# Kernel optimization log

Measured on AMD Instinct MI355X. Metric: run time of the kernel, lower is better.

Reference implementation:

```python
import jax, jax.numpy as jnp
import numpy as np

EMB_DIM = 1024
HEAD_SIZE = 128
B, T = 8, 2048


def setup_inputs() -> dict:
    key = jax.random.key(0)
    kx, kk, kq, kv = jax.random.split(key, 4)
    x = jax.random.normal(kx, (B, T, EMB_DIM), dtype=jnp.float32)
    # torch nn.Linear(emb_dim, head_size, bias=False): weight [head_size, emb_dim], y = x @ W.T
    # store transposed as [emb_dim, head_size] for direct matmul
    s = 1.0 / np.sqrt(EMB_DIM)
    Wk = jax.random.uniform(kk, (EMB_DIM, HEAD_SIZE), dtype=jnp.float32, minval=-s, maxval=s)
    Wq = jax.random.uniform(kq, (EMB_DIM, HEAD_SIZE), dtype=jnp.float32, minval=-s, maxval=s)
    Wv = jax.random.uniform(kv, (EMB_DIM, HEAD_SIZE), dtype=jnp.float32, minval=-s, maxval=s)
    return {"x": x, "Wk": Wk, "Wq": Wq, "Wv": Wv}


def reference(x, Wk, Wq, Wv):
    Bb, Tt, C = x.shape
    k = jnp.einsum('btc,ch->bth', x, Wk)
    q = jnp.einsum('btc,ch->bth', x, Wq)
    v = jnp.einsum('btc,ch->bth', x, Wv)
    # NOTE: original computes k @ q^T (not q @ k^T) and scales by C**-0.5 (C = emb_dim)
    wei = jnp.einsum('bih,bjh->bij', k, q) * (C ** -0.5)  # [B, T, T]
    causal = jnp.tril(jnp.ones((Tt, Tt), dtype=bool))
    wei = jnp.where(causal, wei, -jnp.inf)
    wei = jax.nn.softmax(wei, axis=-1)
    out = jnp.einsum('bij,bjh->bih', wei, v)  # [B, T, head_size]
    return out
```

## Files before the change

### kernel.cpp

```cpp
#include <hip/hip_runtime.h>
#include <hip/hip_bf16.h>
#include <stdint.h>

#define Bn 8
#define Tn 2048
#define Cn 1024
#define Hn 128

typedef __attribute__((ext_vector_type(8))) short short8;
typedef __attribute__((ext_vector_type(4))) short short4v;
typedef __attribute__((ext_vector_type(4))) float f32x4;
typedef __attribute__((ext_vector_type(4))) int int4v;

static __device__ __forceinline__ unsigned short f2bf(float f) {
    union { float f; unsigned int u; } v; v.f = f;
    return (unsigned short)((v.u + 0x7FFFu + ((v.u >> 16) & 1u)) >> 16);
}
static __device__ __forceinline__ float bf2f(unsigned short h) {
    union { unsigned int u; float f; } v; v.u = ((unsigned int)h) << 16;
    return v.f;
}

static __device__ __forceinline__ short8 cvt8(f32x4 a, f32x4 b) {
    union { unsigned int u[4]; short8 s; } r;
    asm("v_cvt_pk_bf16_f32 %0, %1, %2" : "=v"(r.u[0]) : "v"(a[0]), "v"(a[1]));
    asm("v_cvt_pk_bf16_f32 %0, %1, %2" : "=v"(r.u[1]) : "v"(a[2]), "v"(a[3]));
    asm("v_cvt_pk_bf16_f32 %0, %1, %2" : "=v"(r.u[2]) : "v"(b[0]), "v"(b[1]));
    asm("v_cvt_pk_bf16_f32 %0, %1, %2" : "=v"(r.u[3]) : "v"(b[2]), "v"(b[3]));
    return r.s;
}

static __device__ __forceinline__ void async16(const void* g, void* l) {
    __builtin_amdgcn_global_load_lds(
        (const __attribute__((address_space(1))) unsigned int*)g,
        (__attribute__((address_space(3))) unsigned int*)l,
        16, 0, 0);
}

#define KSCALE 0.04508422f

#define BASE_BYTES (3u * Bn * Tn * Hn * 2u + 3u * Hn * Cn * 2u)
#define SLOT_SH 2080
#define NBLK_FA 576
#define UPB_FA 72
#define CCHUNK 8

__global__ __launch_bounds__(256) void wt_prep(const float* __restrict__ Wk,
                                               const float* __restrict__ Wq,
                                               const float* __restrict__ Wv,
                                               unsigned short* __restrict__ WT) {
    int z = blockIdx.y;
    const float* W = (z == 0) ? Wk : (z == 1) ? Wq : Wv;
    unsigned short* wt = WT + (size_t)z * Hn * Cn;
    int o = blockIdx.x * 256 + threadIdx.x;
    int d = o >> 10;
    int k = o & (Cn - 1);
    wt[o] = f2bf(W[k * Hn + d]);
}

__global__ __launch_bounds__(256) void proj6(const float* __restrict__ x,
                                             const unsigned short* __restrict__ WTb,
                                             unsigned short* __restrict__ Kb,
                                             unsigned short* __restrict__ Qb,
                                             unsigned short* __restrict__ VT) {
    __shared__ __align__(16) unsigned short Bsm[2][128 * 32];
    __shared__ __align__(16) float Asm[2][64 * 32];
    int tid = threadIdx.x;
    int lane = tid & 63, w = tid >> 6;
    int lr = lane & 15, lg = lane >> 4;
    int wm = w >> 1, wn = w & 1;

    int u = ((int)(blockIdx.x & 7)) * 96 + ((int)blockIdx.x >> 3);
    int rg = u / 3, cg = u - rg * 3;
    int r0 = rg * 64;
    const unsigned short* WTz = WTb + (size_t)cg * Hn * Cn;

    int br_in = lane >> 2;
    int bc8 = (lane & 3) * 8;
    int ar_in = lane >> 3;
    int aspos = lane & 7;

    auto STAGE = [&](int bb, int k0) {
        #pragma unroll
        for (int i = 0; i < 2; ++i) {
            int ch = w * 2 + i;
            int brow = ch * 16 + br_in;
            async16(WTz + (size_t)brow * Cn + k0 + bc8, &Bsm[bb][ch * 512]);
            int arow = ch * 8 + ar_in;
            int ac = aspos ^ (arow & 7);
            async16(x + (size_t)(r0 + arow) * Cn + k0 + ac * 4, &Asm[bb][ch * 256]);
        }
    };

    f32x4 acc[2][4] = {};
    STAGE(0, 0);
    __syncthreads();
    int cur = 0;
    for (int ks = 0; ks < 32; ++ks) {
        if (ks < 31) STAGE(cur ^ 1, (ks + 1) * 32);
        short8 af[2], bf[4];
        #pragma unroll
        for (int m = 0; m < 2; ++m) {
            int arow = wm * 32 + m * 16 + lr;
            const char* abase = (const char*)&Asm[cur][arow * 32];
            f32x4 a0 = *(const f32x4*)(abase + ((((lg * 2)    ) ^ (arow & 7)) << 4));
            f32x4 a1 = *(const f32x4*)(abase + ((((lg * 2) + 1) ^ (arow & 7)) << 4));
            af[m] = cvt8(a0, a1);
        }
        #pragma unroll
        for (int c = 0; c < 4; ++c) {
            int brow = wn * 64 + c * 16 + lr;
            bf[c] = *(const short8*)(&Bsm[cur][brow * 32 + lg * 8]);
        }
        #pragma unroll
        for (int m = 0; m < 2; ++m)
            #pragma unroll
            for (int c = 0; c < 4; ++c)
                acc[m][c] = __builtin_amdgcn_mfma_f32_16x16x32_bf16(af[m], bf[c], acc[m][c], 0, 0, 0);
        __syncthreads();
        cur ^= 1;
    }

    if (cg == 2) {
        int bb = r0 >> 11;
        int tb = r0 & 2047;
        #pragma unroll
        for (int m = 0; m < 2; ++m)
            #pragma unroll
            for (int c = 0; c < 4; ++c) {
                int d = wn * 64 + c * 16 + lr;
                int t = tb + wm * 32 + m * 16 + lg * 4;
                short4v pv;
                pv[0] = (short)f2bf(acc[m][c][0]);
                pv[1] = (short)f2bf(acc[m][c][1]);
                pv[2] = (short)f2bf(acc[m][c][2]);
                pv[3] = (short)f2bf(acc[m][c][3]);
                *(short4v*)(VT + ((size_t)(bb * Hn + d) << 11) + t) = pv;
            }
    } else {
        unsigned short* outp = (cg == 0) ? Kb : Qb;
        float sc = (cg == 0) ? KSCALE : 1.0f;
        #pragma unroll
        for (int m = 0; m < 2; ++m)
            #pragma unroll
            for (int c = 0; c < 4; ++c) {
                int d = wn * 64 + c * 16 + lr;
                #pragma unroll
                for (int r = 0; r < 4; ++r) {
                    int i = r0 + wm * 32 + m * 16 + lg * 4 + r;
                    outp[(size_t)i * Hn + d] = f2bf(acc[m][c][r] * sc);
                }
            }
    }
}

__global__ __launch_bounds__(512) void fattn8(const unsigned short* __restrict__ Kb,
                                              const unsigned short* __restrict__ Qb,
                                              const unsigned short* __restrict__ VT,
                                              unsigned short* __restrict__ accP) {
    __shared__ __align__(16) unsigned short Ksm[2][32 * 128];
    __shared__ __align__(16) unsigned short Vsm[2][128 * 32];
    __shared__ __align__(16) unsigned short pbuf[8][16][48];
    int tid = threadIdx.x, lane = tid & 63, w = tid >> 6;
    int lr = lane & 15, lg = lane >> 4;

    int cpx = gridDim.x >> 3;
    int u = ((int)blockIdx.x & 7) * cpx + ((int)blockIdx.x >> 3);
    int b = u / UPB_FA, rem = u - b * UPB_FA;
    int g = 0, p = 0;
    for (;;) {
        int P = (4 * g + 4 + CCHUNK - 1) / CCHUNK;
        if (rem < P) { p = rem; break; }
        rem -= P; ++g;
    }
    int nt = 4 * g + 4;
    int P = (nt + CCHUNK - 1) / CCHUNK;
    int q = nt / P, r = nt % P;
    int begin = p * q + (p < r ? p : r);
    int size = q + (p < r ? 1 : 0);

    int i0 = g * 128 + w * 16;
    int tmax = (i0 + 15) >> 5;
    const unsigned short* kb = Kb + (size_t)b * Tn * Hn;
    const unsigned short* qb = Qb + (size_t)b * Tn * Hn;
    const unsigned short* vt = VT + (size_t)b * Hn * Tn;

    short8 kf[4];
    #pragma unroll
    for (int kk = 0; kk < 4; ++kk)
        kf[kk] = *(const short8*)(kb + (size_t)(i0 + lr) * Hn + kk * 32 + lg * 8);

    int krow = tid >> 4, kcol = (tid & 15) * 8;
    int vrow = tid >> 2, vcol = (tid & 3) * 8;
    int4v kreg, vreg;
    auto LOADT = [&](int tt) {
        int j0 = tt * 32;
        kreg = *(const int4v*)(qb + (size_t)(j0 + krow) * Hn + kcol);
        vreg = *(const int4v*)(vt + (size_t)vrow * Tn + j0 + vcol);
    };
    auto WRITET = [&](int bb) {
        *(int4v*)((char*)&Ksm[bb][0] + krow * 256 + ((kcol * 2) ^ ((krow & 7) << 4))) = kreg;
        *(int4v*)((char*)&Vsm[bb][0] + vrow * 64 + vcol * 2) = vreg;
    };

    f32x4 acc[8] = {};
    float ssum[4] = {0.f, 0.f, 0.f, 0.f};

    LOADT(begin);
    WRITET(0);
    __syncthreads();
    int cur = 0;
    for (int ti = 0; ti < size; ++ti) {
        int tt = begin + ti;
        if (ti + 1 < size) LOADT(tt + 1);
        if (tt <= tmax) {
            int j0 = tt * 32;
            const char* kbp = (const char*)&Ksm[cur][0];
            const char* vbp = (const char*)&Vsm[cur][0];
            f32x4 sa0 = {}, sa1 = {};
            #pragma unroll
            for (int kk = 0; kk < 4; ++kk) {
                int row = lr;
                short8 qf = *(const short8*)(kbp + row * 256 + (((kk * 64) + lg * 16) ^ ((row & 7) << 4)));
                sa0 = __builtin_amdgcn_mfma_f32_16x16x32_bf16(kf[kk], qf, sa0, 0, 0, 0);
            }
            #pragma unroll
            for (int kk = 0; kk < 4; ++kk) {
                int row = 16 + lr;
                short8 qf = *(const short8*)(kbp + row * 256 + (((kk * 64) + lg * 16) ^ ((row & 7) << 4)));
                sa1 = __builtin_amdgcn_mfma_f32_16x16x32_bf16(kf[kk], qf, sa1, 0, 0, 0);
            }
            bool needmask = (j0 + 31 > i0);
            #pragma unroll
            for (int rr = 0; rr < 4; ++rr) {
                float v0 = sa0[rr], v1 = sa1[rr];
                if (needmask) {
                    int i = i0 + lg * 4 + rr;
                    if (j0 + lr > i)      v0 = -1e30f;
                    if (j0 + 16 + lr > i) v1 = -1e30f;
                }
                float p0 = __builtin_amdgcn_exp2f(v0);
                float p1 = __builtin_amdgcn_exp2f(v1);
                ssum[rr] += p0 + p1;
                pbuf[w][lg * 4 + rr][lr] = f2bf(p0);
                pbuf[w][lg * 4 + rr][16 + lr] = f2bf(p1);
            }
            short8 pf = *(const short8*)(&pbuf[w][lr][lg * 8]);
            #pragma unroll
            for (int n = 0; n < 8; ++n) {
                int row = n * 16 + lr;
                short8 vf = *(const short8*)(vbp + row * 64 + lg * 16);
                acc[n] = __builtin_amdgcn_mfma_f32_16x16x32_bf16(pf, vf, acc[n], 0, 0, 0);
            }
        }
        if (ti + 1 < size) WRITET(cur ^ 1);
        __syncthreads();
        cur ^= 1;
    }

    unsigned short* dst = accP + (size_t)u * 8 * SLOT_SH + (size_t)w * SLOT_SH;
    #pragma unroll
    for (int n = 0; n < 8; ++n) {
        short4v pv;
        pv[0] = (short)f2bf(acc[n][0]);
        pv[1] = (short)f2bf(acc[n][1]);
        pv[2] = (short)f2bf(acc[n][2]);
        pv[3] = (short)f2bf(acc[n][3]);
        *(short4v*)(dst + n * 256 + lane * 4) = pv;
    }
    #pragma unroll
    for (int rr = 0; rr < 4; ++rr) {
        float s = ssum[rr];
        s += __shfl_xor(s, 1);
        s += __shfl_xor(s, 2);
        s += __shfl_xor(s, 4);
        s += __shfl_xor(s, 8);
        if (lr == 0) ((float*)(dst + 2048))[lg * 4 + rr] = s;
    }
}

__global__ __launch_bounds__(256) void combine3(const unsigned short* __restrict__ accP,
                                                float* __restrict__ out) {
    int cpx = gridDim.x >> 3;
    int bidx = ((int)blockIdx.x & 7) * cpx + ((int)blockIdx.x >> 3);
    int b = bidx >> 7, tile = bidx & 127;
    int g = tile >> 3, wq = tile & 7;
    int ub = b * UPB_FA;
    for (int gg = 0; gg < g; ++gg) ub += (4 * gg + 4 + CCHUNK - 1) / CCHUNK;
    int nt = 4 * g + 4;
    int P = (nt + CCHUNK - 1) / CCHUNK;

    int tid = threadIdx.x;
    int row = tid >> 4;
    int c8 = (tid & 15) * 8;

    const unsigned short* base = accP + ((size_t)ub * 8 + wq) * SLOT_SH;
    const size_t pstr = (size_t)8 * SLOT_SH;
    float den = 0.f;
    for (int pp = 0; pp < P; ++pp) den += ((const float*)(base + pp * pstr + 2048))[row];
    float inv = 1.0f / den;

    int lgg = row >> 2, r4 = row & 3;
    float ov[8];
    #pragma unroll
    for (int cc = 0; cc < 8; ++cc) {
        int col = c8 + cc;
        int n = col >> 4, lrr = col & 15;
        int flat = n * 256 + (lgg * 16 + lrr) * 4 + r4;
        float s = 0.f;
        for (int pp = 0; pp < P; ++pp) s += bf2f(base[pp * pstr + flat]);
        ov[cc] = s * inv;
    }
    float* op = out + ((size_t)(b * Tn + tile * 16 + row)) * Hn + c8;
    *(f32x4*)op       = f32x4{ov[0], ov[1], ov[2], ov[3]};
    *(f32x4*)(op + 4) = f32x4{ov[4], ov[5], ov[6], ov[7]};
}

__global__ __launch_bounds__(256) void attn(const unsigned short* __restrict__ Kb,
                                            const unsigned short* __restrict__ Qb,
                                            const unsigned short* __restrict__ VT,
                                            float* __restrict__ out) {
    __shared__ unsigned short pbuf[4][16][32];
    __shared__ __align__(16) float accbuf[4][16][132];
    __shared__ float ssbuf[4][16];
    int lane = threadIdx.x & 63;
    int w = threadIdx.x >> 6;
    int b = blockIdx.y;
    int xb = blockIdx.x;
    int tile = (xb & 1) ? (127 - (xb >> 1)) : (xb >> 1);
    int i0 = tile * 16;
    int lr = lane & 15, lg = lane >> 4;

    const unsigned short* kb = Kb + (size_t)b * Tn * Hn;
    const unsigned short* qb = Qb + (size_t)b * Tn * Hn;
    const unsigned short* vt = VT + (size_t)b * Hn * Tn;

    short8 kf[4];
    #pragma unroll
    for (int kk = 0; kk < 4; ++kk)
        kf[kk] = *(const short8*)(kb + (size_t)(i0 + lr) * Hn + kk * 32 + lg * 8);

    f32x4 acc[8] = {};
    float ssum[4] = {0.f, 0.f, 0.f, 0.f};

    int nt = (i0 + 15) / 32 + 1;
    for (int tt = w; tt < nt; tt += 4) {
        int j0 = tt * 32;
        f32x4 sa0 = {}, sa1 = {};
        #pragma unroll
        for (int kk = 0; kk < 4; ++kk) {
            short8 q0 = *(const short8*)(qb + (size_t)(j0 + lr) * Hn + kk * 32 + lg * 8);
            sa0 = __builtin_amdgcn_mfma_f32_16x16x32_bf16(kf[kk], q0, sa0, 0, 0, 0);
        }
        #pragma unroll
        for (int kk = 0; kk < 4; ++kk) {
            short8 q1 = *(const short8*)(qb + (size_t)(j0 + 16 + lr) * Hn + kk * 32 + lg * 8);
            sa1 = __builtin_amdgcn_mfma_f32_16x16x32_bf16(kf[kk], q1, sa1, 0, 0, 0);
        }
        bool needmask = (j0 + 31 > i0);
        #pragma unroll
        for (int r = 0; r < 4; ++r) {
            float v0 = sa0[r], v1 = sa1[r];
            if (needmask) {
                int i = i0 + lg * 4 + r;
                if (j0 + lr > i)      v0 = -1e30f;
                if (j0 + 16 + lr > i) v1 = -1e30f;
            }
            float p0 = __builtin_amdgcn_exp2f(v0);
            float p1 = __builtin_amdgcn_exp2f(v1);
            ssum[r] += p0 + p1;
            pbuf[w][lg * 4 + r][lr] = f2bf(p0);
            pbuf[w][lg * 4 + r][16 + lr] = f2bf(p1);
        }
        short8 pf = *(const short8*)(&pbuf[w][lr][lg * 8]);
        #pragma unroll
        for (int n = 0; n < 8; ++n) {
            short8 vf = *(const short8*)(vt + (size_t)(n * 16 + lr) * Tn + j0 + lg * 8);
            acc[n] = __builtin_amdgcn_mfma_f32_16x16x32_bf16(pf, vf, acc[n], 0, 0, 0);
        }
    }

    #pragma unroll
    for (int r = 0; r < 4; ++r) {
        float s = ssum[r];
        s += __shfl_xor(s, 1);
        s += __shfl_xor(s, 2);
        s += __shfl_xor(s, 4);
        s += __shfl_xor(s, 8);
        if (lr == 0) ssbuf[w][lg * 4 + r] = s;
    }
    #pragma unroll
    for (int n = 0; n < 8; ++n)
        #pragma unroll
        for (int r = 0; r < 4; ++r)
            accbuf[w][lg * 4 + r][n * 16 + lr] = acc[n][r];
    __syncthreads();

    int row = threadIdx.x >> 5;
    int col = (threadIdx.x & 31) * 4;
    #pragma unroll
    for (int h = 0; h < 2; ++h) {
        int rr = row + h * 8;
        f32x4 s = *(const f32x4*)(&accbuf[0][rr][col]);
        #pragma unroll
        for (int ww = 1; ww < 4; ++ww) {
            f32x4 t = *(const f32x4*)(&accbuf[ww][rr][col]);
            s[0] += t[0]; s[1] += t[1]; s[2] += t[2]; s[3] += t[3];
        }
        float den = ssbuf[0][rr] + ssbuf[1][rr] + ssbuf[2][rr] + ssbuf[3][rr];
        float inv = 1.0f / den;
        s[0] *= inv; s[1] *= inv; s[2] *= inv; s[3] *= inv;
        *(f32x4*)(&out[((size_t)(b * Tn + i0 + rr)) * Hn + col]) = s;
    }
}

extern "C" void kernel_launch(void* const* d_in, const int* in_sizes, int n_in,
                              void* d_out, int out_size, void* d_ws, size_t ws_size,
                              hipStream_t stream) {
    const float* x  = (const float*)d_in[0];
    const float* Wk = (const float*)d_in[1];
    const float* Wq = (const float*)d_in[2];
    const float* Wv = (const float*)d_in[3];

    unsigned short* Kb = (unsigned short*)d_ws;
    unsigned short* Qb = Kb + (size_t)Bn * Tn * Hn;
    unsigned short* VT = Qb + (size_t)Bn * Tn * Hn;
    unsigned short* WT = VT + (size_t)Bn * Tn * Hn;
    unsigned short* accP = (unsigned short*)((char*)d_ws + BASE_BYTES);

    wt_prep<<<dim3(512, 3), 256, 0, stream>>>(Wk, Wq, Wv, WT);
    proj6<<<dim3(768), 256, 0, stream>>>(x, WT, Kb, Qb, VT);

    const size_t need = (size_t)BASE_BYTES + (size_t)NBLK_FA * 8 * SLOT_SH * 2;
    if (ws_size >= need) {
        fattn8<<<dim3(NBLK_FA), 512, 0, stream>>>(Kb, Qb, VT, accP);
        combine3<<<dim3(1024), 256, 0, stream>>>(accP, (float*)d_out);
    } else {
        attn<<<dim3(128, 8), 256, 0, stream>>>(Kb, Qb, VT, (float*)d_out);
    }
}
```

Baseline: 83.47 us.

## Load x via registers, convert to bf16 once into LDS, double K-step to 64

```diff
diff --git a/kernel.cpp b/kernel.cpp
--- a/kernel.cpp
+++ b/kernel.cpp
@@ -58,13 +58,13 @@
     wt[o] = f2bf(W[k * Hn + d]);
 }
 
-__global__ __launch_bounds__(256) void proj6(const float* __restrict__ x,
+__global__ __launch_bounds__(256) void proj7(const float* __restrict__ x,
                                              const unsigned short* __restrict__ WTb,
                                              unsigned short* __restrict__ Kb,
                                              unsigned short* __restrict__ Qb,
                                              unsigned short* __restrict__ VT) {
-    __shared__ __align__(16) unsigned short Bsm[2][128 * 32];
-    __shared__ __align__(16) float Asm[2][64 * 32];
+    __shared__ __align__(16) unsigned short Bsm[2][128 * 64];
+    __shared__ __align__(16) unsigned short Asm[2][64 * 64];
     int tid = threadIdx.x;
     int lane = tid & 63, w = tid >> 6;
     int lr = lane & 15, lg = lane >> 4;
@@ -75,48 +75,74 @@
     int r0 = rg * 64;
     const unsigned short* WTz = WTb + (size_t)cg * Hn * Cn;
 
-    int br_in = lane >> 2;
-    int bc8 = (lane & 3) * 8;
-    int ar_in = lane >> 3;
-    int aspos = lane & 7;
-
-    auto STAGE = [&](int bb, int k0) {
-        #pragma unroll
-        for (int i = 0; i < 2; ++i) {
-            int ch = w * 2 + i;
-            int brow = ch * 16 + br_in;
-            async16(WTz + (size_t)brow * Cn + k0 + bc8, &Bsm[bb][ch * 512]);
-            int arow = ch * 8 + ar_in;
-            int ac = aspos ^ (arow & 7);
-            async16(x + (size_t)(r0 + arow) * Cn + k0 + ac * 4, &Asm[bb][ch * 256]);
-        }
+    int brow_in = lane >> 3;
+    int bslot = (lane & 7) ^ brow_in;
+    const unsigned short* bsrc[4];
+    #pragma unroll
+    for (int i = 0; i < 4; ++i) {
+        int ch = w * 4 + i;
+        bsrc[i] = WTz + (size_t)(ch * 8 + brow_in) * Cn + bslot * 8;
+    }
+
+    int ar_s = tid >> 2;
+    int ah = tid & 3;
+    const float* axp = x + (size_t)(r0 + ar_s) * Cn + ah * 16;
+    int asw = (ar_s & 7) << 4;
+    unsigned int awb0 = ar_s * 128 + ((ah * 32) ^ asw);
+    unsigned int awb1 = ar_s * 128 + ((ah * 32 + 16) ^ asw);
+
+    f32x4 a_r[4];
+    auto LOADA = [&](int k0) {
+        #pragma unroll
+        for (int i = 0; i < 4; ++i)
+            a_r[i] = *(const f32x4*)(axp + k0 + i * 4);
     };
+    auto STAGEB = [&](int bb, int k0) {
+        #pragma unroll
+        for (int i = 0; i < 4; ++i)
+            async16(bsrc[i] + k0, &Bsm[bb][(w * 4 + i) * 512]);
+    };
+    auto WRITEA = [&](int bb) {
+        short8 w0 = cvt8(a_r[0], a_r[1]);
+        short8 w1 = cvt8(a_r[2], a_r[3]);
+        char* base = (char*)&Asm[bb][0];
+        *(short8*)(base + awb0) = w0;
+        *(short8*)(base + awb1) = w1;
+    };
 
     f32x4 acc[2][4] = {};
-    STAGE(0, 0);
+    LOADA(0);
+    STAGEB(0, 0);
+    WRITEA(0);
     __syncthreads();
     int cur = 0;
-    for (int ks = 0; ks < 32; ++ks) {
-        if (ks < 31) STAGE(cur ^ 1, (ks + 1) * 32);
-        short8 af[2], bf[4];
-        #pragma unroll
-        for (int m = 0; m < 2; ++m) {
-            int arow = wm * 32 + m * 16 + lr;
-            const char* abase = (const char*)&Asm[cur][arow * 32];
-            f32x4 a0 = *(const f32x4*)(abase + ((((lg * 2)    ) ^ (arow & 7)) << 4));
-            f32x4 a1 = *(const f32x4*)(abase + ((((lg * 2) + 1) ^ (arow & 7)) << 4));
-            af[m] = cvt8(a0, a1);
-        }
-        #pragma unroll
-        for (int c = 0; c < 4; ++c) {
-            int brow = wn * 64 + c * 16 + lr;
-            bf[c] = *(const short8*)(&Bsm[cur][brow * 32 + lg * 8]);
-        }
-        #pragma unroll
-        for (int m = 0; m < 2; ++m)
-            #pragma unroll
-            for (int c = 0; c < 4; ++c)
-                acc[m][c] = __builtin_amdgcn_mfma_f32_16x16x32_bf16(af[m], bf[c], acc[m][c], 0, 0, 0);
+    for (int ks = 0; ks < 16; ++ks) {
+        if (ks < 15) {
+            LOADA((ks + 1) * 64);
+            STAGEB(cur ^ 1, (ks + 1) * 64);
+        }
+        const char* ab = (const char*)&Asm[cur][0];
+        const char* bbp = (const char*)&Bsm[cur][0];
+        #pragma unroll
+        for (int kk = 0; kk < 2; ++kk) {
+            short8 af[2], bf[4];
+            #pragma unroll
+            for (int m = 0; m < 2; ++m) {
+                int row = wm * 32 + m * 16 + lr;
+                af[m] = *(const short8*)(ab + row * 128 + ((kk * 64 + lg * 16) ^ ((row & 7) << 4)));
+            }
+            #pragma unroll
+            for (int c = 0; c < 4; ++c) {
+                int row = wn * 64 + c * 16 + lr;
+                bf[c] = *(const short8*)(bbp + row * 128 + ((kk * 64 + lg * 16) ^ ((row & 7) << 4)));
+            }
+            #pragma unroll
+            for (int m = 0; m < 2; ++m)
+                #pragma unroll
+                for (int c = 0; c < 4; ++c)
+                    acc[m][c] = __builtin_amdgcn_mfma_f32_16x16x32_bf16(af[m], bf[c], acc[m][c], 0, 0, 0);
+        }
+        if (ks < 15) WRITEA(cur ^ 1);
         __syncthreads();
         cur ^= 1;
     }
@@ -429,7 +455,7 @@
     unsigned short* accP = (unsigned short*)((char*)d_ws + BASE_BYTES);
 
     wt_prep<<<dim3(512, 3), 256, 0, stream>>>(Wk, Wq, Wv, WT);
-    proj6<<<dim3(768), 256, 0, stream>>>(x, WT, Kb, Qb, VT);
+    proj7<<<dim3(768), 256, 0, stream>>>(x, WT, Kb, Qb, VT);
 
     const size_t need = (size_t)BASE_BYTES + (size_t)NBLK_FA * 8 * SLOT_SH * 2;
     if (ws_size >= need) {
```

Result: no change. 83.93 us (+0.6%).

## Triple-buffer projection GEMM with vmcnt waits and swizzled B tile

Applied to the files above, without the earlier changes.

```diff
diff --git a/kernel.cpp b/kernel.cpp
--- a/kernel.cpp
+++ b/kernel.cpp
@@ -58,13 +58,13 @@
     wt[o] = f2bf(W[k * Hn + d]);
 }
 
-__global__ __launch_bounds__(256) void proj6(const float* __restrict__ x,
+__global__ __launch_bounds__(256) void proj9(const float* __restrict__ x,
                                              const unsigned short* __restrict__ WTb,
                                              unsigned short* __restrict__ Kb,
                                              unsigned short* __restrict__ Qb,
                                              unsigned short* __restrict__ VT) {
-    __shared__ __align__(16) unsigned short Bsm[2][128 * 32];
-    __shared__ __align__(16) float Asm[2][64 * 32];
+    __shared__ __align__(16) unsigned short Bsm[3][128 * 32];
+    __shared__ __align__(16) float Asm[3][64 * 32];
     int tid = threadIdx.x;
     int lane = tid & 63, w = tid >> 6;
     int lr = lane & 15, lg = lane >> 4;
@@ -75,50 +75,63 @@
     int r0 = rg * 64;
     const unsigned short* WTz = WTb + (size_t)cg * Hn * Cn;
 
-    int br_in = lane >> 2;
-    int bc8 = (lane & 3) * 8;
-    int ar_in = lane >> 3;
-    int aspos = lane & 7;
+    const unsigned short* bsrc[2];
+    const float* asrc[2];
+    #pragma unroll
+    for (int i = 0; i < 2; ++i) {
+        int ch = w * 2 + i;
+        int brow = ch * 16 + (lane >> 2);
+        int bslot = (lane & 3) ^ ((brow >> 1) & 3);
+        bsrc[i] = WTz + (size_t)brow * Cn + bslot * 8;
+        int arow = ch * 8 + (lane >> 3);
+        int aslot = (lane & 7) ^ (arow & 7);
+        asrc[i] = x + (size_t)(r0 + arow) * Cn + aslot * 4;
+    }
 
     auto STAGE = [&](int bb, int k0) {
         #pragma unroll
         for (int i = 0; i < 2; ++i) {
             int ch = w * 2 + i;
-            int brow = ch * 16 + br_in;
-            async16(WTz + (size_t)brow * Cn + k0 + bc8, &Bsm[bb][ch * 512]);
-            int arow = ch * 8 + ar_in;
-            int ac = aspos ^ (arow & 7);
-            async16(x + (size_t)(r0 + arow) * Cn + k0 + ac * 4, &Asm[bb][ch * 256]);
+            async16(bsrc[i] + k0, &Bsm[bb][ch * 512]);
+            async16(asrc[i] + k0, &Asm[bb][ch * 256]);
         }
     };
 
     f32x4 acc[2][4] = {};
     STAGE(0, 0);
-    __syncthreads();
+    STAGE(1, 32);
     int cur = 0;
     for (int ks = 0; ks < 32; ++ks) {
-        if (ks < 31) STAGE(cur ^ 1, (ks + 1) * 32);
+        if (ks < 31) asm volatile("s_waitcnt vmcnt(4)" ::: "memory");
+        else         asm volatile("s_waitcnt vmcnt(0)" ::: "memory");
+        __builtin_amdgcn_s_barrier();
+        __builtin_amdgcn_sched_barrier(0);
+        if (ks < 30) {
+            int nb = cur + 2; if (nb >= 3) nb -= 3;
+            STAGE(nb, (ks + 2) * 32);
+        }
+        const char* ab = (const char*)&Asm[cur][0];
+        const char* bbp = (const char*)&Bsm[cur][0];
         short8 af[2], bf[4];
         #pragma unroll
         for (int m = 0; m < 2; ++m) {
-            int arow = wm * 32 + m * 16 + lr;
-            const char* abase = (const char*)&Asm[cur][arow * 32];
-            f32x4 a0 = *(const f32x4*)(abase + ((((lg * 2)    ) ^ (arow & 7)) << 4));
-            f32x4 a1 = *(const f32x4*)(abase + ((((lg * 2) + 1) ^ (arow & 7)) << 4));
+            int row = wm * 32 + m * 16 + lr;
+            const char* abase = ab + row * 128;
+            f32x4 a0 = *(const f32x4*)(abase + (((lg * 2)     ^ (row & 7)) << 4));
+            f32x4 a1 = *(const f32x4*)(abase + (((lg * 2 + 1) ^ (row & 7)) << 4));
             af[m] = cvt8(a0, a1);
         }
         #pragma unroll
         for (int c = 0; c < 4; ++c) {
-            int brow = wn * 64 + c * 16 + lr;
-            bf[c] = *(const short8*)(&Bsm[cur][brow * 32 + lg * 8]);
+            int row = wn * 64 + c * 16 + lr;
+            bf[c] = *(const short8*)(bbp + row * 64 + ((lg ^ ((row >> 1) & 3)) << 4));
         }
         #pragma unroll
         for (int m = 0; m < 2; ++m)
             #pragma unroll
             for (int c = 0; c < 4; ++c)
                 acc[m][c] = __builtin_amdgcn_mfma_f32_16x16x32_bf16(af[m], bf[c], acc[m][c], 0, 0, 0);
-        __syncthreads();
-        cur ^= 1;
+        ++cur; if (cur == 3) cur = 0;
     }
 
     if (cg == 2) {
@@ -429,7 +442,7 @@
     unsigned short* accP = (unsigned short*)((char*)d_ws + BASE_BYTES);
 
     wt_prep<<<dim3(512, 3), 256, 0, stream>>>(Wk, Wq, Wv, WT);
-    proj6<<<dim3(768), 256, 0, stream>>>(x, WT, Kb, Qb, VT);
+    proj9<<<dim3(768), 256, 0, stream>>>(x, WT, Kb, Qb, VT);
 
     const size_t need = (size_t)BASE_BYTES + (size_t)NBLK_FA * 8 * SLOT_SH * 2;
     if (ws_size >= need) {
```

Result: no change. 83.01 us (median of 3 runs) (-0.6%).

## Fuse K/Q/V projections into one 64x384 tile per block to reuse x

Applied to the files above, without the earlier changes.

```diff
diff --git a/kernel.cpp b/kernel.cpp
--- a/kernel.cpp
+++ b/kernel.cpp
@@ -58,77 +58,89 @@
     wt[o] = f2bf(W[k * Hn + d]);
 }
 
-__global__ __launch_bounds__(256) void proj6(const float* __restrict__ x,
-                                             const unsigned short* __restrict__ WTb,
-                                             unsigned short* __restrict__ Kb,
-                                             unsigned short* __restrict__ Qb,
-                                             unsigned short* __restrict__ VT) {
-    __shared__ __align__(16) unsigned short Bsm[2][128 * 32];
-    __shared__ __align__(16) float Asm[2][64 * 32];
+__global__ __launch_bounds__(512) void proj10(const float* __restrict__ x,
+                                              const unsigned short* __restrict__ WTb,
+                                              unsigned short* __restrict__ Kb,
+                                              unsigned short* __restrict__ Qb,
+                                              unsigned short* __restrict__ VT) {
+    __shared__ __align__(16) unsigned short Bsm[2][384 * 64];
+    __shared__ __align__(16) float Asm[2][64 * 64];
     int tid = threadIdx.x;
     int lane = tid & 63, w = tid >> 6;
     int lr = lane & 15, lg = lane >> 4;
-    int wm = w >> 1, wn = w & 1;
-
-    int u = ((int)(blockIdx.x & 7)) * 96 + ((int)blockIdx.x >> 3);
-    int rg = u / 3, cg = u - rg * 3;
-    int r0 = rg * 64;
-    const unsigned short* WTz = WTb + (size_t)cg * Hn * Cn;
-
-    int br_in = lane >> 2;
-    int bc8 = (lane & 3) * 8;
-    int ar_in = lane >> 3;
-    int aspos = lane & 7;
+    int wm = w >> 2, wn = w & 3;
+
+    int u = ((int)(blockIdx.x & 7)) * 32 + ((int)blockIdx.x >> 3);
+    int r0 = u * 64;
+
+    const unsigned short* bsrcp[6];
+    #pragma unroll
+    for (int i = 0; i < 6; ++i) {
+        int brow = (w * 6 + i) * 8 + (lane >> 3);
+        int bslot = (lane & 7) ^ (brow & 7);
+        bsrcp[i] = WTb + (size_t)brow * Cn + bslot * 8;
+    }
+    const float* asrcp[2];
+    #pragma unroll
+    for (int i = 0; i < 2; ++i) {
+        int arow = (w * 2 + i) * 4 + (lane >> 4);
+        int aslot = (lane & 15) ^ (arow & 7);
+        asrcp[i] = x + (size_t)(r0 + arow) * Cn + aslot * 4;
+    }
 
     auto STAGE = [&](int bb, int k0) {
         #pragma unroll
-        for (int i = 0; i < 2; ++i) {
-            int ch = w * 2 + i;
-            int brow = ch * 16 + br_in;
-            async16(WTz + (size_t)brow * Cn + k0 + bc8, &Bsm[bb][ch * 512]);
-            int arow = ch * 8 + ar_in;
-            int ac = aspos ^ (arow & 7);
-            async16(x + (size_t)(r0 + arow) * Cn + k0 + ac * 4, &Asm[bb][ch * 256]);
-        }
+        for (int i = 0; i < 6; ++i)
+            async16(bsrcp[i] + k0, &Bsm[bb][(w * 6 + i) * 512]);
+        #pragma unroll
+        for (int i = 0; i < 2; ++i)
+            async16(asrcp[i] + k0, &Asm[bb][(w * 2 + i) * 256]);
     };
 
-    f32x4 acc[2][4] = {};
+    f32x4 acc[2][6] = {};
     STAGE(0, 0);
     __syncthreads();
     int cur = 0;
-    for (int ks = 0; ks < 32; ++ks) {
-        if (ks < 31) STAGE(cur ^ 1, (ks + 1) * 32);
-        short8 af[2], bf[4];
-        #pragma unroll
-        for (int m = 0; m < 2; ++m) {
-            int arow = wm * 32 + m * 16 + lr;
-            const char* abase = (const char*)&Asm[cur][arow * 32];
-            f32x4 a0 = *(const f32x4*)(abase + ((((lg * 2)    ) ^ (arow & 7)) << 4));
-            f32x4 a1 = *(const f32x4*)(abase + ((((lg * 2) + 1) ^ (arow & 7)) << 4));
-            af[m] = cvt8(a0, a1);
-        }
-        #pragma unroll
-        for (int c = 0; c < 4; ++c) {
-            int brow = wn * 64 + c * 16 + lr;
-            bf[c] = *(const short8*)(&Bsm[cur][brow * 32 + lg * 8]);
-        }
-        #pragma unroll
-        for (int m = 0; m < 2; ++m)
-            #pragma unroll
-            for (int c = 0; c < 4; ++c)
-                acc[m][c] = __builtin_amdgcn_mfma_f32_16x16x32_bf16(af[m], bf[c], acc[m][c], 0, 0, 0);
+    for (int ks = 0; ks < 16; ++ks) {
+        if (ks < 15) STAGE(cur ^ 1, (ks + 1) * 64);
+        const char* ab = (const char*)&Asm[cur][0];
+        const char* bbp = (const char*)&Bsm[cur][0];
+        #pragma unroll
+        for (int kk = 0; kk < 2; ++kk) {
+            short8 af[2], bf[6];
+            #pragma unroll
+            for (int m = 0; m < 2; ++m) {
+                int row = wm * 32 + m * 16 + lr;
+                const char* abase = ab + row * 256;
+                f32x4 a0 = *(const f32x4*)(abase + (((kk * 8 + lg * 2)     ^ (row & 7)) << 4));
+                f32x4 a1 = *(const f32x4*)(abase + (((kk * 8 + lg * 2 + 1) ^ (row & 7)) << 4));
+                af[m] = cvt8(a0, a1);
+            }
+            #pragma unroll
+            for (int c = 0; c < 6; ++c) {
+                int row = wn * 96 + c * 16 + lr;
+                bf[c] = *(const short8*)(bbp + row * 128 + (((kk * 4 + lg) ^ (row & 7)) << 4));
+            }
+            #pragma unroll
+            for (int m = 0; m < 2; ++m)
+                #pragma unroll
+                for (int c = 0; c < 6; ++c)
+                    acc[m][c] = __builtin_amdgcn_mfma_f32_16x16x32_bf16(af[m], bf[c], acc[m][c], 0, 0, 0);
+        }
         __syncthreads();
         cur ^= 1;
     }
 
-    if (cg == 2) {
-        int bb = r0 >> 11;
-        int tb = r0 & 2047;
-        #pragma unroll
-        for (int m = 0; m < 2; ++m)
-            #pragma unroll
-            for (int c = 0; c < 4; ++c) {
-                int d = wn * 64 + c * 16 + lr;
+    int bb = r0 >> 11;
+    int tb = r0 & 2047;
+    #pragma unroll
+    for (int m = 0; m < 2; ++m)
+        #pragma unroll
+        for (int c = 0; c < 6; ++c) {
+            int col0 = wn * 96 + c * 16;
+            int z = col0 >> 7;
+            int d = (col0 & 127) + lr;
+            if (z == 2) {
                 int t = tb + wm * 32 + m * 16 + lg * 4;
                 short4v pv;
                 pv[0] = (short)f2bf(acc[m][c][0]);
@@ -136,22 +148,16 @@
                 pv[2] = (short)f2bf(acc[m][c][2]);
                 pv[3] = (short)f2bf(acc[m][c][3]);
                 *(short4v*)(VT + ((size_t)(bb * Hn + d) << 11) + t) = pv;
-            }
-    } else {
-        unsigned short* outp = (cg == 0) ? Kb : Qb;
-        float sc = (cg == 0) ? KSCALE : 1.0f;
-        #pragma unroll
-        for (int m = 0; m < 2; ++m)
-            #pragma unroll
-            for (int c = 0; c < 4; ++c) {
-                int d = wn * 64 + c * 16 + lr;
+            } else {
+                unsigned short* outp = (z == 0) ? Kb : Qb;
+                float sc = (z == 0) ? KSCALE : 1.0f;
                 #pragma unroll
                 for (int r = 0; r < 4; ++r) {
                     int i = r0 + wm * 32 + m * 16 + lg * 4 + r;
                     outp[(size_t)i * Hn + d] = f2bf(acc[m][c][r] * sc);
                 }
             }
-    }
+        }
 }
 
 __global__ __launch_bounds__(512) void fattn8(const unsigned short* __restrict__ Kb,
@@ -429,7 +435,7 @@
     unsigned short* accP = (unsigned short*)((char*)d_ws + BASE_BYTES);
 
     wt_prep<<<dim3(512, 3), 256, 0, stream>>>(Wk, Wq, Wv, WT);
-    proj6<<<dim3(768), 256, 0, stream>>>(x, WT, Kb, Qb, VT);
+    proj10<<<dim3(256), 512, 0, stream>>>(x, WT, Kb, Qb, VT);
 
     const size_t need = (size_t)BASE_BYTES + (size_t)NBLK_FA * 8 * SLOT_SH * 2;
     if (ws_size >= need) {
```

Result: slower. 85.87 us (+2.9%).
